# Kernel tuning notes

Measured on AMD Instinct MI355X. Metric: run time of the kernel, lower is better.

## Reference

```python
import jax, jax.numpy as jnp
import numpy as np

H = 2048      # hidden_size
NH = 32       # num attention heads
KVH = 8       # num kv heads
HD = 64       # head_dim
G = NH // KVH # kv groups (4)
EPS = 1e-6
THETA = 1000000.0


def _rms_norm(x, g):
    # normalize over last dim (head_dim)
    var = jnp.mean(jnp.square(x), axis=-1, keepdims=True)
    return x * jax.lax.rsqrt(var + EPS) * g


def _rope(seq_len, dtype):
    inv_freq = 1.0 / (THETA ** (jnp.arange(0, HD, 2, dtype=jnp.float32) / HD))
    pos = jnp.arange(seq_len, dtype=jnp.float32)
    freqs = pos[:, None] * inv_freq[None, :]          # [S, HD/2]
    emb = jnp.concatenate([freqs, freqs], axis=-1)    # [S, HD]
    return jnp.cos(emb).astype(dtype), jnp.sin(emb).astype(dtype)


def _rotate_half(x):
    x1, x2 = jnp.split(x, 2, axis=-1)
    return jnp.concatenate([-x2, x1], axis=-1)


def setup_inputs() -> dict:
    key = jax.random.key(0)
    ks = jax.random.split(key, 8)
    B, S = 1, 2048
    s = lambda fan_in: 1.0 / np.sqrt(fan_in)
    return {
        "hidden_states": jax.random.normal(ks[0], (B, S, H), jnp.float32),
        "Wq": jax.random.normal(ks[1], (H, NH * HD + NH), jnp.float32) * s(H),
        "Wk": jax.random.normal(ks[2], (H, KVH * HD), jnp.float32) * s(H),
        "Wv": jax.random.normal(ks[3], (H, KVH * HD), jnp.float32) * s(H),
        "Wo": jax.random.normal(ks[4], (NH * HD, H), jnp.float32) * s(NH * HD),
        "g_q": jnp.ones((HD,), jnp.float32),
        "g_k": jnp.ones((HD,), jnp.float32),
    }


def reference(hidden_states, Wq, Wk, Wv, Wo, g_q, g_k):
    B, S, _ = hidden_states.shape
    dtype = hidden_states.dtype

    qg = hidden_states @ Wq                              # [B,S,NH*HD+NH]
    k = hidden_states @ Wk                               # [B,S,KVH*HD]
    v = hidden_states @ Wv

    # headwise gate split, grouped per kv head (matches torch view/split)
    qg = qg.reshape(B, S, KVH, G * HD + G)
    q, gate = qg[..., : G * HD], qg[..., G * HD :]       # gate: [B,S,KVH,G]
    gate = gate.reshape(B, S, NH, 1)
    q = q.reshape(B, S, NH, HD).transpose(0, 2, 1, 3)    # [B,NH,S,HD]
    k = k.reshape(B, S, KVH, HD).transpose(0, 2, 1, 3)   # [B,KVH,S,HD]
    v = v.reshape(B, S, KVH, HD).transpose(0, 2, 1, 3)

    q = _rms_norm(q, g_q)
    k = _rms_norm(k, g_k)

    cos, sin = _rope(S, dtype)                           # [S,HD]
    cos, sin = cos[None, None], sin[None, None]
    q = q * cos + _rotate_half(q) * sin
    k = k * cos + _rotate_half(k) * sin

    # GQA: repeat kv heads
    k = jnp.repeat(k, G, axis=1)                         # [B,NH,S,HD]
    v = jnp.repeat(v, G, axis=1)

    # causal SDPA
    scale = 1.0 / np.sqrt(HD)
    scores = jnp.einsum("bhqd,bhkd->bhqk", q, k) * scale
    causal = jnp.tril(jnp.ones((S, S), bool))
    scores = jnp.where(causal[None, None], scores, jnp.finfo(dtype).min)
    probs = jax.nn.softmax(scores, axis=-1)
    attn = jnp.einsum("bhqk,bhkd->bhqd", probs, v)       # [B,NH,S,HD]

    attn = attn.transpose(0, 2, 1, 3)                    # [B,S,NH,HD]
    attn = attn * jax.nn.sigmoid(gate)
    attn = attn.reshape(B, S, NH * HD)
    return attn @ Wo
```

## Files before the change

kernel.cpp:

```cpp
#include <hip/hip_runtime.h>
#include <hip/hip_bf16.h>

#define SLEN 2048
#define HDIM 2048
#define NHEAD 32
#define KVHEAD 8
#define HEADD 64
#define NTOT 3104
#define NPAD 3200

typedef short bh8 __attribute__((ext_vector_type(8)));
typedef float f32x4 __attribute__((ext_vector_type(4)));

#define QSCALE 0.1803368801111204f

__device__ __forceinline__ unsigned short f2bf(float f) {
    union { float f; unsigned int u; } v; v.f = f;
    unsigned int u = v.u;
    return (unsigned short)((u + 0x7fffu + ((u >> 16) & 1u)) >> 16);
}

__device__ __forceinline__ unsigned int cvtpk_bf16(float lo, float hi) {
    unsigned int r;
    asm("v_cvt_pk_bf16_f32 %0, %1, %2" : "=v"(r) : "v"(lo), "v"(hi));
    return r;
}

__device__ __forceinline__ void gl_lds16(const unsigned short* g, unsigned short* l) {
    __builtin_amdgcn_global_load_lds(
        (const __attribute__((address_space(1))) unsigned int*)g,
        (__attribute__((address_space(3))) unsigned int*)l, 16, 0, 0);
}

__global__ void cast_x_k(const float* __restrict__ src, unsigned short* __restrict__ dst, int n) {
    int i = blockIdx.x * blockDim.x + threadIdx.x;
    int base = i * 4;
    if (base < n) {
        float4 f = *(const float4*)(src + base);
        ushort4 o;
        o.x = f2bf(f.x); o.y = f2bf(f.y); o.z = f2bf(f.z); o.w = f2bf(f.w);
        *(ushort4*)(dst + base) = o;
    }
}

__global__ void pack_wt_k(const float* __restrict__ Wq, const float* __restrict__ Wk,
                          const float* __restrict__ Wv, unsigned short* __restrict__ Wt) {
    __shared__ float tile[32][33];
    int n0 = blockIdx.x * 32, k0 = blockIdx.y * 32;
    int t = threadIdx.x;
    for (int i = 0; i < 4; i++) {
        int idx = i * 256 + t;
        int kr = idx >> 5, nc = idx & 31;
        int n = n0 + nc, k = k0 + kr;
        float val = 0.f;
        if (n < 2048)       { int h = n >> 6, d = n & 63; val = Wq[(size_t)k * 2080 + (h >> 2) * 260 + (h & 3) * 64 + d]; }
        else if (n < 2080)  { int h = n - 2048;           val = Wq[(size_t)k * 2080 + (h >> 2) * 260 + 256 + (h & 3)]; }
        else if (n < 2592)  { val = Wk[(size_t)k * 512 + (n - 2080)]; }
        else if (n < 3104)  { val = Wv[(size_t)k * 512 + (n - 2592)]; }
        tile[kr][nc] = val;
    }
    __syncthreads();
    for (int i = 0; i < 4; i++) {
        int idx = i * 256 + t;
        int nr = idx >> 5, kc = idx & 31;
        Wt[(size_t)(n0 + nr) * HDIM + (k0 + kc)] = f2bf(tile[kc][nr]);
    }
}

__global__ void pack_wot_k(const float* __restrict__ Wo, unsigned short* __restrict__ Wt) {
    __shared__ float tile[32][33];
    int n0 = blockIdx.x * 32, k0 = blockIdx.y * 32;
    int t = threadIdx.x;
    for (int i = 0; i < 4; i++) {
        int idx = i * 256 + t;
        int kr = idx >> 5, nc = idx & 31;
        tile[kr][nc] = Wo[(size_t)(k0 + kr) * 2048 + (n0 + nc)];
    }
    __syncthreads();
    for (int i = 0; i < 4; i++) {
        int idx = i * 256 + t;
        int nr = idx >> 5, kc = idx & 31;
        Wt[(size_t)(n0 + nr) * 2048 + (k0 + kc)] = f2bf(tile[kc][nr]);
    }
}

__global__ __launch_bounds__(256) void gemm_nt_k(const unsigned short* __restrict__ A,
                                                 const unsigned short* __restrict__ Bt,
                                                 float* __restrict__ C,
                                                 int K, int ldc) {
    __shared__ unsigned short As[128 * 32];
    __shared__ unsigned short Bs[128 * 32];
    int d = blockIdx.y * gridDim.x + blockIdx.x;
    int nwg = gridDim.x * gridDim.y;
    int cpx = nwg >> 3;
    int swz = (d & 7) * cpx + (d >> 3);
    int m0 = (swz % gridDim.x) * 128, n0 = (swz / gridDim.x) * 128;
    int t = threadIdx.x;
    int w = t >> 6, l = t & 63;
    int wm = (w >> 1) * 64, wn = (w & 1) * 64;
    int lrow = l & 15, lk = (l >> 4) * 8;
    int srowA = (w * 2) * 16 + (l >> 2);
    int scol = (l & 3) * 8;

    f32x4 acc[4][4];
    #pragma unroll
    for (int i = 0; i < 4; i++)
        #pragma unroll
        for (int j = 0; j < 4; j++)
            acc[i][j] = {0.f, 0.f, 0.f, 0.f};

    for (int k0 = 0; k0 < K; k0 += 32) {
        const unsigned short* ga0 = &A[(size_t)(m0 + srowA) * K + k0 + scol];
        const unsigned short* gb0 = &Bt[(size_t)(n0 + srowA) * K + k0 + scol];
        gl_lds16(ga0,                  &As[(w * 2 + 0) * 512]);
        gl_lds16(ga0 + 16 * (size_t)K, &As[(w * 2 + 1) * 512]);
        gl_lds16(gb0,                  &Bs[(w * 2 + 0) * 512]);
        gl_lds16(gb0 + 16 * (size_t)K, &Bs[(w * 2 + 1) * 512]);
        __syncthreads();
        bh8 af[4], bb[4];
        #pragma unroll
        for (int i = 0; i < 4; i++) {
            af[i] = *(const bh8*)(&As[(wm + i * 16 + lrow) * 32 + lk]);
            bb[i] = *(const bh8*)(&Bs[(wn + i * 16 + lrow) * 32 + lk]);
        }
        #pragma unroll
        for (int i = 0; i < 4; i++)
            #pragma unroll
            for (int j = 0; j < 4; j++)
                acc[i][j] = __builtin_amdgcn_mfma_f32_16x16x32_bf16(af[i], bb[j], acc[i][j], 0, 0, 0);
        __syncthreads();
    }
    int col = l & 15, rbase = (l >> 4) * 4;
    for (int i = 0; i < 4; i++)
        for (int j = 0; j < 4; j++)
            #pragma unroll
            for (int r = 0; r < 4; r++)
                C[(size_t)(m0 + wm + i * 16 + rbase + r) * ldc + (n0 + wn + j * 16 + col)] = acc[i][j][r];
}

__global__ __launch_bounds__(256) void gemm_nt64_k(const unsigned short* __restrict__ A,
                                                   const unsigned short* __restrict__ Bt,
                                                   float* __restrict__ C) {
    const int K = 2048, ldc = 2048;
    __shared__ unsigned short As[64 * 32];
    __shared__ unsigned short Bs[128 * 32];
    int d = blockIdx.x;
    int swz = (d & 7) * 64 + (d >> 3);
    int m0 = (swz & 31) * 64, n0 = (swz >> 5) * 128;
    int t = threadIdx.x;
    int w = t >> 6, l = t & 63;
    int wm = (w >> 1) * 32, wn = (w & 1) * 64;
    int lrow = l & 15, lk = (l >> 4) * 8;
    int srow = (l >> 2), scol = (l & 3) * 8;

    f32x4 acc[2][4];
    #pragma unroll
    for (int i = 0; i < 2; i++)
        #pragma unroll
        for (int j = 0; j < 4; j++)
            acc[i][j] = {0.f, 0.f, 0.f, 0.f};

    for (int k0 = 0; k0 < K; k0 += 32) {
        gl_lds16(&A[(size_t)(m0 + w * 16 + srow) * K + k0 + scol], &As[w * 512]);
        gl_lds16(&Bt[(size_t)(n0 + (w * 2 + 0) * 16 + srow) * K + k0 + scol], &Bs[(w * 2 + 0) * 512]);
        gl_lds16(&Bt[(size_t)(n0 + (w * 2 + 1) * 16 + srow) * K + k0 + scol], &Bs[(w * 2 + 1) * 512]);
        __syncthreads();
        bh8 af[2], bb[4];
        #pragma unroll
        for (int i = 0; i < 2; i++)
            af[i] = *(const bh8*)(&As[(wm + i * 16 + lrow) * 32 + lk]);
        #pragma unroll
        for (int j = 0; j < 4; j++)
            bb[j] = *(const bh8*)(&Bs[(wn + j * 16 + lrow) * 32 + lk]);
        #pragma unroll
        for (int i = 0; i < 2; i++)
            #pragma unroll
            for (int j = 0; j < 4; j++)
                acc[i][j] = __builtin_amdgcn_mfma_f32_16x16x32_bf16(af[i], bb[j], acc[i][j], 0, 0, 0);
        __syncthreads();
    }
    int col = l & 15, rbase = (l >> 4) * 4;
    for (int i = 0; i < 2; i++)
        for (int j = 0; j < 4; j++)
            #pragma unroll
            for (int r = 0; r < 4; r++)
                C[(size_t)(m0 + wm + i * 16 + rbase + r) * ldc + (n0 + wn + j * 16 + col)] = acc[i][j][r];
}

__global__ void norm_rope_k(const float* __restrict__ QKVG, unsigned short* __restrict__ Qr,
                            unsigned short* __restrict__ Kr,
                            const float* __restrict__ g_q, const float* __restrict__ g_k) {
    int wid = blockIdx.x * (blockDim.x >> 6) + (threadIdx.x >> 6);
    int lane = threadIdx.x & 63;
    int type, s, hh;
    if (wid < SLEN * NHEAD) { type = 0; s = wid >> 5; hh = wid & 31; }
    else                    { int r = wid - SLEN * NHEAD; type = 1; s = r >> 3; hh = r & 7; }
    int col = (type == 0) ? hh * 64 + lane : 2080 + hh * 64 + lane;
    float x = QKVG[(size_t)s * NPAD + col];
    float sq = x * x;
    #pragma unroll
    for (int off = 32; off; off >>= 1) sq += __shfl_xor(sq, off);
    float inv = rsqrtf(sq * (1.f / 64.f) + 1e-6f);
    float g = (type == 0 ? g_q : g_k)[lane];
    float xn = x * inv * g;
    float xp = __shfl_xor(xn, 32);
    float xr = (lane < 32) ? -xp : xp;
    int i = lane & 31;
    float invf = __expf(-(float)i * (0.03125f * 13.815510557964274f));
    float ang = (float)s * invf;
    float c = cosf(ang), sn = sinf(ang);
    float r = xn * c + xr * sn;
    if (type == 0) Qr[((size_t)hh * SLEN + s) * 64 + lane] = f2bf(r * QSCALE);
    else           Kr[((size_t)hh * SLEN + s) * 64 + lane] = f2bf(r);
}

__global__ void vt_k(const float* __restrict__ QKVG, unsigned short* __restrict__ Vt) {
    __shared__ float tile[64][65];
    int s0 = blockIdx.x * 64, hh = blockIdx.y;
    int t = threadIdx.x;
    #pragma unroll
    for (int i = 0; i < 4; i++) {
        int idx = i * 256 + t;
        int sr = idx >> 4, c4 = (idx & 15) * 4;
        float4 f = *(const float4*)(&QKVG[(size_t)(s0 + sr) * NPAD + 2592 + hh * 64 + c4]);
        tile[sr][c4] = f.x; tile[sr][c4 + 1] = f.y; tile[sr][c4 + 2] = f.z; tile[sr][c4 + 3] = f.w;
    }
    __syncthreads();
    #pragma unroll
    for (int i = 0; i < 4; i++) {
        int idx = i * 256 + t;
        int dr = idx >> 4, c4 = (idx & 15) * 4;
        int hb = c4 >> 5, f = (c4 >> 4) & 1, g = (c4 >> 2) & 3;
        int p = (hb * 4 + g) * 8 + f * 4;
        ushort4 o;
        o.x = f2bf(tile[c4][dr]); o.y = f2bf(tile[c4 + 1][dr]);
        o.z = f2bf(tile[c4 + 2][dr]); o.w = f2bf(tile[c4 + 3][dr]);
        *(ushort4*)(&Vt[((size_t)hh * 64 + dr) * SLEN + s0 + p]) = o;
    }
}

__global__ void gate_sig_k(const float* __restrict__ QKVG, float* __restrict__ gate) {
    int i = blockIdx.x * 256 + threadIdx.x;
    int s = i >> 5, h = i & 31;
    float x = QKVG[(size_t)s * NPAD + 2048 + h];
    gate[i] = 1.f / (1.f + __expf(-x));
}

__global__ __launch_bounds__(256) void attn_k(const unsigned short* __restrict__ Qr,
                                              const unsigned short* __restrict__ Kr,
                                              const unsigned short* __restrict__ Vt,
                                              const float* __restrict__ gate,
                                              unsigned short* __restrict__ attn) {
    __shared__ unsigned short Kls[3][64 * 64];
    __shared__ unsigned short Vls[3][64 * 64];
    int d = blockIdx.y * gridDim.x + blockIdx.x;
    int kvh = d & 7;
    int j8 = d >> 3;
    int h = kvh * 4 + (j8 >> 4);
    int xp = j8 & 15;
    int t = threadIdx.x, w = t >> 6, l = t & 63;
    int ql = l & 15, g = l >> 4;
    const float NEGINF = -__builtin_inff();

    const unsigned short* Kh = Kr + (size_t)kvh * SLEN * 64;
    const unsigned short* Vh = Vt + (size_t)kvh * 64 * SLEN;
    const unsigned short* Qh = Qr + (size_t)h * SLEN * 64;
    int lk = g * 8;
    int r8 = l >> 3, c8 = l & 7;
    int cs = 8 * (c8 ^ r8);
    int R0 = w * 16, R1 = w * 16 + 8;
    int rdswz = (ql & 7) << 4;

    for (int half = 0; half < 2; half++) {
        int qt = half ? 31 - xp : xp;
        int q0 = qt * 64;
        int qrow = q0 + w * 16 + ql;

        bh8 qa0 = *(const bh8*)(Qh + (size_t)qrow * 64 + lk);
        bh8 qa1 = *(const bh8*)(Qh + (size_t)qrow * 64 + 32 + lk);

        f32x4 o[4];
        #pragma unroll
        for (int i = 0; i < 4; i++) o[i] = {0.f, 0.f, 0.f, 0.f};
        float m2 = NEGINF, lsum = 0.f;

        int ntiles = qt + 1;
        {
            gl_lds16(&Kh[(size_t)(0 + R0 + r8) * 64 + cs], &Kls[0][R0 * 64]);
            gl_lds16(&Kh[(size_t)(0 + R1 + r8) * 64 + cs], &Kls[0][R1 * 64]);
            gl_lds16(&Vh[(size_t)(R0 + r8) * SLEN + 0 + cs], &Vls[0][R0 * 64]);
            gl_lds16(&Vh[(size_t)(R1 + r8) * SLEN + 0 + cs], &Vls[0][R1 * 64]);
        }
        if (ntiles > 1) {
            gl_lds16(&Kh[(size_t)(64 + R0 + r8) * 64 + cs], &Kls[1][R0 * 64]);
            gl_lds16(&Kh[(size_t)(64 + R1 + r8) * 64 + cs], &Kls[1][R1 * 64]);
            gl_lds16(&Vh[(size_t)(R0 + r8) * SLEN + 64 + cs], &Vls[1][R0 * 64]);
            gl_lds16(&Vh[(size_t)(R1 + r8) * SLEN + 64 + cs], &Vls[1][R1 * 64]);
        }
        int rd = 0, wr = 2;

        for (int ti = 0; ti < ntiles; ti++) {
            if (ti + 1 < ntiles) asm volatile("s_waitcnt vmcnt(4)\n\ts_barrier" ::: "memory");
            else                 asm volatile("s_waitcnt vmcnt(0)\n\ts_barrier" ::: "memory");
            if (ti + 2 < ntiles) {
                int kv1 = (ti + 2) * 64;
                gl_lds16(&Kh[(size_t)(kv1 + R0 + r8) * 64 + cs], &Kls[wr][R0 * 64]);
                gl_lds16(&Kh[(size_t)(kv1 + R1 + r8) * 64 + cs], &Kls[wr][R1 * 64]);
                gl_lds16(&Vh[(size_t)(R0 + r8) * SLEN + kv1 + cs], &Vls[wr][R0 * 64]);
                gl_lds16(&Vh[(size_t)(R1 + r8) * SLEN + kv1 + cs], &Vls[wr][R1 * 64]);
            }
            const unsigned short* Kb = &Kls[rd][0];
            const unsigned short* Vb = &Vls[rd][0];
            int kv0 = ti * 64;
            f32x4 sct[4];
            #pragma unroll
            for (int nt = 0; nt < 4; nt++) {
                int rb = (nt * 16 + ql) * 128;
                bh8 kb0 = *(const bh8*)(&Kb[(rb + ((g * 16) ^ rdswz)) >> 1]);
                bh8 kb1 = *(const bh8*)(&Kb[(rb + ((64 + g * 16) ^ rdswz)) >> 1]);
                f32x4 a = {0.f, 0.f, 0.f, 0.f};
                a = __builtin_amdgcn_mfma_f32_16x16x32_bf16(kb0, qa0, a, 0, 0, 0);
                a = __builtin_amdgcn_mfma_f32_16x16x32_bf16(kb1, qa1, a, 0, 0, 0);
                sct[nt] = a;
            }
            if (ti == qt) {
                #pragma unroll
                for (int nt = 0; nt < 4; nt++)
                    #pragma unroll
                    for (int j = 0; j < 4; j++) {
                        int key = kv0 + nt * 16 + 4 * g + j;
                        if (key > qrow) sct[nt][j] = NEGINF;
                    }
            }
            float mt0 = fmaxf(fmaxf(sct[0][0], sct[0][1]), fmaxf(sct[0][2], sct[0][3]));
            float mt1 = fmaxf(fmaxf(sct[1][0], sct[1][1]), fmaxf(sct[1][2], sct[1][3]));
            float mt2 = fmaxf(fmaxf(sct[2][0], sct[2][1]), fmaxf(sct[2][2], sct[2][3]));
            float mt3 = fmaxf(fmaxf(sct[3][0], sct[3][1]), fmaxf(sct[3][2], sct[3][3]));
            float mt = fmaxf(fmaxf(mt0, mt1), fmaxf(mt2, mt3));
            mt = fmaxf(mt, __shfl_xor(mt, 16));
            mt = fmaxf(mt, __shfl_xor(mt, 32));
            if (!__all(mt - m2 <= 8.f)) {
                float mnew = fmaxf(m2, mt);
                float resc = __builtin_amdgcn_exp2f(m2 - mnew);
                m2 = mnew;
                lsum *= resc;
                float rf[4];
                #pragma unroll
                for (int j = 0; j < 4; j++) rf[j] = __shfl(resc, 4 * g + j);
                #pragma unroll
                for (int nt = 0; nt < 4; nt++) {
                    f32x4 oo = o[nt];
                    #pragma unroll
                    for (int j = 0; j < 4; j++) oo[j] *= rf[j];
                    o[nt] = oo;
                }
            }
            float ps = 0.f;
            #pragma unroll
            for (int nt = 0; nt < 4; nt++)
                #pragma unroll
                for (int j = 0; j < 4; j++) {
                    float p = __builtin_amdgcn_exp2f(sct[nt][j] - m2);
                    sct[nt][j] = p;
                    ps += p;
                }
            ps += __shfl_xor(ps, 16);
            ps += __shfl_xor(ps, 32);
            lsum += ps;
            union { unsigned int u[4]; bh8 v; } pa0, pa1;
            pa0.u[0] = cvtpk_bf16(sct[0][0], sct[0][1]);
            pa0.u[1] = cvtpk_bf16(sct[0][2], sct[0][3]);
            pa0.u[2] = cvtpk_bf16(sct[1][0], sct[1][1]);
            pa0.u[3] = cvtpk_bf16(sct[1][2], sct[1][3]);
            pa1.u[0] = cvtpk_bf16(sct[2][0], sct[2][1]);
            pa1.u[1] = cvtpk_bf16(sct[2][2], sct[2][3]);
            pa1.u[2] = cvtpk_bf16(sct[3][0], sct[3][1]);
            pa1.u[3] = cvtpk_bf16(sct[3][2], sct[3][3]);
            #pragma unroll
            for (int nt = 0; nt < 4; nt++) {
                int rb = (nt * 16 + ql) * 128;
                bh8 vb0 = *(const bh8*)(&Vb[(rb + ((g * 16) ^ rdswz)) >> 1]);
                bh8 vb1 = *(const bh8*)(&Vb[(rb + ((64 + g * 16) ^ rdswz)) >> 1]);
                o[nt] = __builtin_amdgcn_mfma_f32_16x16x32_bf16(pa0.v, vb0, o[nt], 0, 0, 0);
                o[nt] = __builtin_amdgcn_mfma_f32_16x16x32_bf16(pa1.v, vb1, o[nt], 0, 0, 0);
            }
            rd = (rd == 2) ? 0 : rd + 1;
            wr = (wr == 2) ? 0 : wr + 1;
        }
        asm volatile("s_barrier" ::: "memory");

        float gf[4];
        #pragma unroll
        for (int j = 0; j < 4; j++) {
            float ls = __shfl(lsum, 4 * g + j);
            int row = q0 + w * 16 + 4 * g + j;
            gf[j] = gate[row * 32 + h] / ls;
        }
        #pragma unroll
        for (int j = 0; j < 4; j++) {
            int row = q0 + w * 16 + 4 * g + j;
            #pragma unroll
            for (int nt = 0; nt < 4; nt++)
                attn[(size_t)row * 2048 + h * 64 + nt * 16 + ql] = f2bf(o[nt][j] * gf[j]);
        }
    }
}

extern "C" void kernel_launch(void* const* d_in, const int* in_sizes, int n_in,
                              void* d_out, int out_size, void* d_ws, size_t ws_size,
                              hipStream_t stream) {
    const float* hidden = (const float*)d_in[0];
    const float* Wq = (const float*)d_in[1];
    const float* Wk = (const float*)d_in[2];
    const float* Wv = (const float*)d_in[3];
    const float* Wo = (const float*)d_in[4];
    const float* gq = (const float*)d_in[5];
    const float* gk = (const float*)d_in[6];
    float* out = (float*)d_out;
    char* ws = (char*)d_ws;

    unsigned short* X    = (unsigned short*)(ws + 0);
    unsigned short* Wt   = (unsigned short*)(ws + 8388608);
    float*          QKVG = (float*)(ws + 21495808);
    unsigned short* Qr   = (unsigned short*)(ws + 47710208);
    unsigned short* Kr   = (unsigned short*)(ws + 56098816);
    unsigned short* Vt   = (unsigned short*)(ws + 58195968);
    float*          gate = (float*)(ws + 60293120);
    unsigned short* attn = (unsigned short*)(ws + 60555264);
    unsigned short* Wot  = (unsigned short*)(ws + 68943872);

    cast_x_k<<<dim3(4096), dim3(256), 0, stream>>>(hidden, X, SLEN * HDIM);
    pack_wt_k<<<dim3(100, 64), dim3(256), 0, stream>>>(Wq, Wk, Wv, Wt);
    pack_wot_k<<<dim3(64, 64), dim3(256), 0, stream>>>(Wo, Wot);
    gemm_nt_k<<<dim3(16, 25), dim3(256), 0, stream>>>(X, Wt, QKVG, HDIM, NPAD);
    norm_rope_k<<<dim3(20480), dim3(256), 0, stream>>>(QKVG, Qr, Kr, gq, gk);
    vt_k<<<dim3(32, 8), dim3(256), 0, stream>>>(QKVG, Vt);
    gate_sig_k<<<dim3(256), dim3(256), 0, stream>>>(QKVG, gate);
    attn_k<<<dim3(16, 32), dim3(256), 0, stream>>>(Qr, Kr, Vt, gate, attn);
    gemm_nt64_k<<<dim3(512), dim3(256), 0, stream>>>(attn, Wot, out);
}
```

Baseline: 174.3 us.

## Triple-buffer GEMM LDS staging with async prefetch and XOR-swizzled LDS layout

Both NT GEMM kernels now use three LDS buffers and prefetch two K-steps ahead with direct global-to-LDS loads. A partial vmcnt wait plus a single barrier per step replaces the two __syncthreads, so loads overlap the MFMA work. The column chunk is XOR-swizzled by row, on both the global source side and the LDS read side, to cut LDS bank conflicts on fragment reads. LDS use triples, which may lower occupancy, and correctness now depends on the hand-counted vmcnt values and the swizzle matching on both sides.

```diff
diff --git a/kernel.cpp b/kernel.cpp
--- a/kernel.cpp
+++ b/kernel.cpp
@@ -88,8 +88,8 @@
                                                  const unsigned short* __restrict__ Bt,
                                                  float* __restrict__ C,
                                                  int K, int ldc) {
-    __shared__ unsigned short As[128 * 32];
-    __shared__ unsigned short Bs[128 * 32];
+    __shared__ unsigned short As[3][128 * 32];
+    __shared__ unsigned short Bs[3][128 * 32];
     int d = blockIdx.y * gridDim.x + blockIdx.x;
     int nwg = gridDim.x * gridDim.y;
     int cpx = nwg >> 3;
@@ -98,9 +98,10 @@
     int t = threadIdx.x;
     int w = t >> 6, l = t & 63;
     int wm = (w >> 1) * 64, wn = (w & 1) * 64;
-    int lrow = l & 15, lk = (l >> 4) * 8;
-    int srowA = (w * 2) * 16 + (l >> 2);
-    int scol = (l & 3) * 8;
+    int lrow = l & 15, lc = l >> 4;
+    int rsw = (lrow >> 1) & 3;
+    int srowA = w * 32 + (l >> 2);
+    int scol = ((l & 3) ^ ((l >> 3) & 3)) * 8;
 
     f32x4 acc[4][4];
     #pragma unroll
@@ -109,27 +110,41 @@
         for (int j = 0; j < 4; j++)
             acc[i][j] = {0.f, 0.f, 0.f, 0.f};
 
-    for (int k0 = 0; k0 < K; k0 += 32) {
-        const unsigned short* ga0 = &A[(size_t)(m0 + srowA) * K + k0 + scol];
-        const unsigned short* gb0 = &Bt[(size_t)(n0 + srowA) * K + k0 + scol];
-        gl_lds16(ga0,                  &As[(w * 2 + 0) * 512]);
-        gl_lds16(ga0 + 16 * (size_t)K, &As[(w * 2 + 1) * 512]);
-        gl_lds16(gb0,                  &Bs[(w * 2 + 0) * 512]);
-        gl_lds16(gb0 + 16 * (size_t)K, &Bs[(w * 2 + 1) * 512]);
-        __syncthreads();
+    const unsigned short* ga = &A[(size_t)(m0 + srowA) * K + scol];
+    const unsigned short* gb = &Bt[(size_t)(n0 + srowA) * K + scol];
+    int nst = K >> 5;
+
+#define STAGE_NT(s, b) do { \
+        const unsigned short* ga0 = ga + (size_t)(s) * 32; \
+        const unsigned short* gb0 = gb + (size_t)(s) * 32; \
+        gl_lds16(ga0,                  &As[b][(w * 2 + 0) * 512]); \
+        gl_lds16(ga0 + 16 * (size_t)K, &As[b][(w * 2 + 1) * 512]); \
+        gl_lds16(gb0,                  &Bs[b][(w * 2 + 0) * 512]); \
+        gl_lds16(gb0 + 16 * (size_t)K, &Bs[b][(w * 2 + 1) * 512]); \
+    } while (0)
+
+    STAGE_NT(0, 0);
+    STAGE_NT(1, 1);
+    int rd = 0, wr = 2;
+    for (int s = 0; s < nst; s++) {
+        if (s + 1 < nst) asm volatile("s_waitcnt vmcnt(4)\n\ts_barrier" ::: "memory");
+        else             asm volatile("s_waitcnt vmcnt(0)\n\ts_barrier" ::: "memory");
+        if (s + 2 < nst) STAGE_NT(s + 2, wr);
         bh8 af[4], bb[4];
         #pragma unroll
         for (int i = 0; i < 4; i++) {
-            af[i] = *(const bh8*)(&As[(wm + i * 16 + lrow) * 32 + lk]);
-            bb[i] = *(const bh8*)(&Bs[(wn + i * 16 + lrow) * 32 + lk]);
+            af[i] = *(const bh8*)(&As[rd][(wm + i * 16 + lrow) * 32 + ((lc ^ rsw) * 8)]);
+            bb[i] = *(const bh8*)(&Bs[rd][(wn + i * 16 + lrow) * 32 + ((lc ^ rsw) * 8)]);
         }
         #pragma unroll
         for (int i = 0; i < 4; i++)
             #pragma unroll
             for (int j = 0; j < 4; j++)
                 acc[i][j] = __builtin_amdgcn_mfma_f32_16x16x32_bf16(af[i], bb[j], acc[i][j], 0, 0, 0);
-        __syncthreads();
-    }
+        rd = (rd == 2) ? 0 : rd + 1;
+        wr = (wr == 2) ? 0 : wr + 1;
+    }
+#undef STAGE_NT
     int col = l & 15, rbase = (l >> 4) * 4;
     for (int i = 0; i < 4; i++)
         for (int j = 0; j < 4; j++)
@@ -142,16 +157,17 @@
                                                    const unsigned short* __restrict__ Bt,
                                                    float* __restrict__ C) {
     const int K = 2048, ldc = 2048;
-    __shared__ unsigned short As[64 * 32];
-    __shared__ unsigned short Bs[128 * 32];
+    __shared__ unsigned short As[3][64 * 32];
+    __shared__ unsigned short Bs[3][128 * 32];
     int d = blockIdx.x;
     int swz = (d & 7) * 64 + (d >> 3);
     int m0 = (swz & 31) * 64, n0 = (swz >> 5) * 128;
     int t = threadIdx.x;
     int w = t >> 6, l = t & 63;
     int wm = (w >> 1) * 32, wn = (w & 1) * 64;
-    int lrow = l & 15, lk = (l >> 4) * 8;
-    int srow = (l >> 2), scol = (l & 3) * 8;
+    int lrow = l & 15, lc = l >> 4;
+    int rsw = (lrow >> 1) & 3;
+    int scol = ((l & 3) ^ ((l >> 3) & 3)) * 8;
 
     f32x4 acc[2][4];
     #pragma unroll
@@ -160,25 +176,39 @@
         for (int j = 0; j < 4; j++)
             acc[i][j] = {0.f, 0.f, 0.f, 0.f};
 
-    for (int k0 = 0; k0 < K; k0 += 32) {
-        gl_lds16(&A[(size_t)(m0 + w * 16 + srow) * K + k0 + scol], &As[w * 512]);
-        gl_lds16(&Bt[(size_t)(n0 + (w * 2 + 0) * 16 + srow) * K + k0 + scol], &Bs[(w * 2 + 0) * 512]);
-        gl_lds16(&Bt[(size_t)(n0 + (w * 2 + 1) * 16 + srow) * K + k0 + scol], &Bs[(w * 2 + 1) * 512]);
-        __syncthreads();
+    const unsigned short* ga = &A[(size_t)(m0 + w * 16 + (l >> 2)) * K + scol];
+    const unsigned short* gb = &Bt[(size_t)(n0 + w * 32 + (l >> 2)) * K + scol];
+    const int nst = K >> 5;
+
+#define STAGE_NT64(s, b) do { \
+        gl_lds16(ga + (size_t)(s) * 32,                  &As[b][w * 512]); \
+        gl_lds16(gb + (size_t)(s) * 32,                  &Bs[b][(w * 2 + 0) * 512]); \
+        gl_lds16(gb + (size_t)(s) * 32 + 16 * (size_t)K, &Bs[b][(w * 2 + 1) * 512]); \
+    } while (0)
+
+    STAGE_NT64(0, 0);
+    STAGE_NT64(1, 1);
+    int rd = 0, wr = 2;
+    for (int s = 0; s < nst; s++) {
+        if (s + 1 < nst) asm volatile("s_waitcnt vmcnt(3)\n\ts_barrier" ::: "memory");
+        else             asm volatile("s_waitcnt vmcnt(0)\n\ts_barrier" ::: "memory");
+        if (s + 2 < nst) STAGE_NT64(s + 2, wr);
         bh8 af[2], bb[4];
         #pragma unroll
         for (int i = 0; i < 2; i++)
-            af[i] = *(const bh8*)(&As[(wm + i * 16 + lrow) * 32 + lk]);
+            af[i] = *(const bh8*)(&As[rd][(wm + i * 16 + lrow) * 32 + ((lc ^ rsw) * 8)]);
         #pragma unroll
         for (int j = 0; j < 4; j++)
-            bb[j] = *(const bh8*)(&Bs[(wn + j * 16 + lrow) * 32 + lk]);
+            bb[j] = *(const bh8*)(&Bs[rd][(wn + j * 16 + lrow) * 32 + ((lc ^ rsw) * 8)]);
         #pragma unroll
         for (int i = 0; i < 2; i++)
             #pragma unroll
             for (int j = 0; j < 4; j++)
                 acc[i][j] = __builtin_amdgcn_mfma_f32_16x16x32_bf16(af[i], bb[j], acc[i][j], 0, 0, 0);
-        __syncthreads();
-    }
+        rd = (rd == 2) ? 0 : rd + 1;
+        wr = (wr == 2) ? 0 : wr + 1;
+    }
+#undef STAGE_NT64
     int col = l & 15, rbase = (l >> 4) * 4;
     for (int i = 0; i < 2; i++)
         for (int j = 0; j < 4; j++)
```

Result: faster. 170.1 us (-2.4%).
